# Performance work log

Hardware: AMD Instinct MI355X
Metric: run time of the kernel (lower is better)

The kernel has to match this reference:

```python
import jax, jax.numpy as jnp
import numpy as np

B, N, D = 1, 512, 128
KEEP = 0.75
LN_EPS = 1e-5


def _layer_norm(x, g, b):
    mu = jnp.mean(x, axis=-1, keepdims=True)
    var = jnp.mean(jnp.square(x - mu), axis=-1, keepdims=True)
    return (x - mu) * jax.lax.rsqrt(var + LN_EPS) * g + b


def _low_norm_dropout(x, keep_fraction=KEEP):
    # Zero features whose L2 norm over d is below the (1-keep) quantile.
    norms = jnp.linalg.norm(x, axis=-1, keepdims=True)  # [B,N,N,1]
    threshold = jnp.quantile(norms.reshape(-1), 1.0 - keep_fraction)
    mask = (norms >= threshold).astype(x.dtype)
    return x * mask / (keep_fraction + 1e-8)


def _linear(x, w):
    # torch nn.Linear (no bias): y = x @ W^T, W is [out, in]
    return jnp.einsum('bijd,od->bijo', x, w)


def setup_inputs() -> dict:
    key = jax.random.key(0)
    ks = jax.random.split(key, 8)
    scale = float(np.sqrt(6.0 / (2.0 * D)))  # xavier_uniform-ish std
    z = jax.random.normal(ks[0], (B, N, N, D), dtype=jnp.float32)
    w = lambda k: jax.random.uniform(k, (D, D), dtype=jnp.float32, minval=-scale, maxval=scale)
    return {
        'z': z,
        'ln_in_g': jnp.ones((D,), jnp.float32),
        'ln_in_b': jnp.zeros((D,), jnp.float32),
        'w_proj_a': w(ks[1]),
        'w_gate_a': w(ks[2]),
        'w_proj_b': w(ks[3]),
        'w_gate_b': w(ks[4]),
        'w_gate_out': w(ks[5]),
        'ln_out_g': jnp.ones((D,), jnp.float32),
        'ln_out_b': jnp.zeros((D,), jnp.float32),
        'w_proj_out': w(ks[6]),
    }


def reference(z, ln_in_g, ln_in_b, w_proj_a, w_gate_a, w_proj_b, w_gate_b,
              w_gate_out, ln_out_g, ln_out_b, w_proj_out):
    residual = z
    m = _layer_norm(z, ln_in_g, ln_in_b)
    a = jax.nn.sigmoid(_linear(m, w_gate_a)) * _linear(m, w_proj_a)
    b = jax.nn.sigmoid(_linear(m, w_gate_b)) * _linear(m, w_proj_b)
    a = _low_norm_dropout(a)
    b = _low_norm_dropout(b)
    # outgoing triangle update: contract over k axis
    t = jnp.einsum('bikd,bjkd->bijd', a, b)
    t = _layer_norm(t, ln_out_g, ln_out_b)
    gate = jax.nn.sigmoid(_linear(m, w_gate_out))
    out = gate * _linear(t, w_proj_out)
    return residual + out
```

## Files before the change

kernel.cpp:

```cpp
#include <hip/hip_runtime.h>
#include <hip/hip_fp16.h>

typedef unsigned int u32;
typedef unsigned short u16;
typedef __attribute__((ext_vector_type(8))) short short8;
typedef __attribute__((ext_vector_type(8))) _Float16 half8;
typedef __attribute__((ext_vector_type(4))) float f32x4;

#define NN (512*512)
#define RANK 65537u

#define L1A 0
#define L1B 1024
#define L2A 2048
#define L2B 6144
#define L3A 10240
#define L3B 11264
#define SEL1 12288
#define REM1 12290
#define SEL2 12292
#define REM2 12294
#define THRF 12296
#define HTOT 12298


__device__ __forceinline__ float bf2f(u16 h){ return __uint_as_float(((u32)h)<<16); }
__device__ __forceinline__ u16 f2bf(float f){
    u32 u = __float_as_uint(f);
    return (u16)((u + 0x7FFFu + ((u>>16)&1u)) >> 16);
}
__device__ __forceinline__ u16 f2bf_rz(float f){
    return (u16)(__float_as_uint(f) >> 16);
}
__device__ __forceinline__ u16 f2h(float f){ return __half_as_ushort(__float2half_rn(f)); }
__device__ __forceinline__ float h2f(u16 b){ return __half2float(__ushort_as_half(b)); }
__device__ __forceinline__ half8 as_h8(short8 x){ union{short8 s; half8 h;} u; u.s=x; return u.h; }
__device__ __forceinline__ float fsig(float x){ return 1.f/(1.f+__expf(-x)); }

__global__ void k0_init(const float* __restrict__ wga, const float* __restrict__ wpa,
                        const float* __restrict__ wgb, const float* __restrict__ wpb,
                        const float* __restrict__ wgo, const float* __restrict__ wpo,
                        u16* __restrict__ wprep, u32* __restrict__ h)
{
    const int i = blockIdx.x*blockDim.x + threadIdx.x;
    const int stride = gridDim.x*blockDim.x;
    for (int j = i; j < HTOT; j += stride) h[j] = 0;
    for (int j = i; j < 16384; j += stride) {
        const int o = j >> 7, c = j & 127;
        const int dj = (j & ~127) | ((((c>>3) ^ (o&7)) << 3)) | (c & 7);
        const float* ws[4] = {wga, wpa, wgb, wpb};
        #pragma unroll
        for (int L = 0; L < 4; ++L) {
            float x = ws[L][j];
            u16 hb = f2h(x);
            float hf = h2f(hb);
            wprep[(L*3+0)*16384 + dj] = hb;
            wprep[(L*3+1)*16384 + dj] = f2bf(x - hf);
            wprep[(L*3+2)*16384 + dj] = f2bf(hf);
        }
        wprep[12*16384 + dj] = f2h(wgo[j]);
        wprep[13*16384 + dj] = f2bf(wpo[j]);
    }
}

__global__ __launch_bounds__(256,2) void k2_fused(
    const float* __restrict__ z, const float* __restrict__ lng, const float* __restrict__ lnb,
    const u16* __restrict__ wp,
    u16* __restrict__ at, u16* __restrict__ bt,
    float* __restrict__ na, float* __restrict__ nb)
{
    __shared__ u16 smem[32768];
    u16* const s0 = smem;
    u16* const s1 = smem + 16384;
    const int tid = threadIdx.x;
    const int r0 = blockIdx.x * 128;
    const int lane = tid & 63;
    const int wid  = tid >> 6;

    #pragma unroll
    for (int pass = 0; pass < 2; ++pass) {
        const int rl = pass*64 + (tid>>2);
        const int q  = tid & 3;
        const float* zr = z + (size_t)(r0 + rl)*128;
        float v[32];
        float s = 0.f;
        #pragma unroll
        for (int j = 0; j < 8; ++j) {
            float4 f = *(const float4*)(zr + q*4 + j*16);
            v[j*4+0]=f.x; v[j*4+1]=f.y; v[j*4+2]=f.z; v[j*4+3]=f.w;
            s += f.x+f.y+f.z+f.w;
        }
        s += __shfl_xor(s,1); s += __shfl_xor(s,2);
        const float mu = s * (1.f/128.f);
        float vs = 0.f;
        #pragma unroll
        for (int e = 0; e < 32; ++e) { float d = v[e]-mu; vs += d*d; }
        vs += __shfl_xor(vs,1); vs += __shfl_xor(vs,2);
        const float x = vs*(1.f/128.f) + 1e-5f;
        float rstd = rsqrtf(x);
        rstd = rstd*(1.5f - 0.5f*x*rstd*rstd);
        #pragma unroll
        for (int j = 0; j < 8; ++j) {
            const int k = q*4 + j*16;
            float4 g4 = *(const float4*)(lng + k);
            float4 b4 = *(const float4*)(lnb + k);
            float m0 = (v[j*4+0]-mu)*rstd*g4.x + b4.x;
            float m1 = (v[j*4+1]-mu)*rstd*g4.y + b4.y;
            float m2 = (v[j*4+2]-mu)*rstd*g4.z + b4.z;
            float m3 = (v[j*4+3]-mu)*rstd*g4.w + b4.w;
            ushort4 ph, pl;
            ph.x = f2h(m0); pl.x = f2bf_rz(m0 - h2f(ph.x));
            ph.y = f2h(m1); pl.y = f2bf_rz(m1 - h2f(ph.y));
            ph.z = f2h(m2); pl.z = f2bf_rz(m2 - h2f(ph.z));
            ph.w = f2h(m3); pl.w = f2bf_rz(m3 - h2f(ph.w));
            const int blk = j*2 + (q>>1);
            const int addr = rl*128 + ((blk ^ (rl&7))*8) + (q&1)*4;
            *(ushort4*)&s0[addr] = ph;
            *(ushort4*)&s1[addr] = pl;
        }
    }
    __syncthreads();

    const int lrow = lane & 15, lkg = lane >> 4;
    const int rw   = wid * 32;

    short8 ah[2][4], al[2][4], ahb[2][4];
    #pragma unroll
    for (int m = 0; m < 2; ++m)
        #pragma unroll
        for (int ks = 0; ks < 4; ++ks) {
            const int row = rw + m*16 + lrow, blk = ks*4 + lkg;
            const int addr = row*128 + ((blk ^ (row&7))*8);
            ah[m][ks] = *(const short8*)&s0[addr];
            al[m][ks] = *(const short8*)&s1[addr];
            short8 c;
            #pragma unroll
            for (int e = 0; e < 8; ++e) c[e] = (short)f2bf_rz(h2f((u16)ah[m][ks][e]));
            ahb[m][ks] = c;
        }
    __syncthreads();

    f32x4 accG[2][8], accP[2][8];

    auto issue = [&](int buf, int slot){
        const char* src = (const char*)wp + (size_t)slot*32768 + wid*8192 + lane*16;
        u16* dst = smem + buf*16384 + wid*4096;
        #pragma unroll
        for (int i = 0; i < 8; ++i) {
            __builtin_amdgcn_global_load_lds((const u32*)(src + i*1024), (u32*)(dst + i*512), 16, 0, 0);
        }
    };
    auto passF16 = [&](f32x4 (&acc)[2][8], const u16* buf){
        #pragma unroll
        for (int ks = 0; ks < 4; ++ks) {
            const int blk = ks*4 + lkg;
            half8 a0 = as_h8(ah[0][ks]), a1 = as_h8(ah[1][ks]);
            #pragma unroll
            for (int n = 0; n < 8; ++n) {
                const int o = n*16 + lrow;
                half8 bF = as_h8(*(const short8*)&buf[o*128 + ((blk ^ (o&7))*8)]);
                acc[0][n] = __builtin_amdgcn_mfma_f32_16x16x32_f16(a0, bF, acc[0][n], 0,0,0);
                acc[1][n] = __builtin_amdgcn_mfma_f32_16x16x32_f16(a1, bF, acc[1][n], 0,0,0);
            }
        }
    };
    auto passBFhb = [&](f32x4 (&acc)[2][8], const u16* buf){
        #pragma unroll
        for (int ks = 0; ks < 4; ++ks) {
            const int blk = ks*4 + lkg;
            short8 a0 = ahb[0][ks], a1 = ahb[1][ks];
            #pragma unroll
            for (int n = 0; n < 8; ++n) {
                const int o = n*16 + lrow;
                short8 bF = *(const short8*)&buf[o*128 + ((blk ^ (o&7))*8)];
                acc[0][n] = __builtin_amdgcn_mfma_f32_16x16x32_bf16(a0, bF, acc[0][n], 0,0,0);
                acc[1][n] = __builtin_amdgcn_mfma_f32_16x16x32_bf16(a1, bF, acc[1][n], 0,0,0);
            }
        }
    };
    auto passBFal = [&](f32x4 (&acc)[2][8], const u16* buf){
        #pragma unroll
        for (int ks = 0; ks < 4; ++ks) {
            const int blk = ks*4 + lkg;
            short8 a0 = al[0][ks], a1 = al[1][ks];
            #pragma unroll
            for (int n = 0; n < 8; ++n) {
                const int o = n*16 + lrow;
                short8 bF = *(const short8*)&buf[o*128 + ((blk ^ (o&7))*8)];
                acc[0][n] = __builtin_amdgcn_mfma_f32_16x16x32_bf16(a0, bF, acc[0][n], 0,0,0);
                acc[1][n] = __builtin_amdgcn_mfma_f32_16x16x32_bf16(a1, bF, acc[1][n], 0,0,0);
            }
        }
    };
    auto epi = [&](u16* __restrict__ dst, float* __restrict__ nrm){
        float ns[2][4];
        #pragma unroll
        for (int m=0;m<2;++m){ ns[m][0]=0.f; ns[m][1]=0.f; ns[m][2]=0.f; ns[m][3]=0.f; }
        #pragma unroll
        for (int m = 0; m < 2; ++m) {
            const int rb = r0 + rw + m*16 + lkg*4;
            #pragma unroll
            for (int n = 0; n < 8; ++n) {
                const int o = n*16 + lrow;
                ushort4 pk;
                float av;
                av = accP[m][n][0] * fsig(accG[m][n][0]); ns[m][0]+=av*av; pk.x=f2bf(av);
                av = accP[m][n][1] * fsig(accG[m][n][1]); ns[m][1]+=av*av; pk.y=f2bf(av);
                av = accP[m][n][2] * fsig(accG[m][n][2]); ns[m][2]+=av*av; pk.z=f2bf(av);
                av = accP[m][n][3] * fsig(accG[m][n][3]); ns[m][3]+=av*av; pk.w=f2bf(av);
                *(ushort4*)&dst[(size_t)o*NN + rb] = pk;
            }
        }
        #pragma unroll
        for (int m = 0; m < 2; ++m)
            #pragma unroll
            for (int g = 0; g < 4; ++g) {
                float s = ns[m][g];
                s += __shfl_xor(s,1); s += __shfl_xor(s,2); s += __shfl_xor(s,4); s += __shfl_xor(s,8);
                if (lrow == 0) nrm[r0 + rw + m*16 + lkg*4 + g] = sqrtf(s);
            }
    };
    auto zacc = [&](f32x4 (&a)[2][8]){
        #pragma unroll
        for (int m=0;m<2;++m)
            #pragma unroll
            for (int n=0;n<8;++n) a[m][n] = (f32x4){0.f,0.f,0.f,0.f};
    };

    u16* const b0 = smem;
    u16* const b1 = smem + 16384;
    issue(0, 0);

#define K2_STEP(I, BODY)                                             \
    issue(((I)+1)&1, (I)+1);                                         \
    asm volatile("s_waitcnt vmcnt(8)" ::: "memory");                 \
    __builtin_amdgcn_sched_barrier(0);                               \
    __builtin_amdgcn_s_barrier();                                    \
    __builtin_amdgcn_s_setprio(1);                                   \
    BODY                                                             \
    __builtin_amdgcn_s_setprio(0);                                   \
    asm volatile("s_waitcnt lgkmcnt(0)" ::: "memory");               \
    __builtin_amdgcn_sched_barrier(0);                               \
    __builtin_amdgcn_s_barrier();

    K2_STEP(0,  { zacc(accG); passF16(accG, b0); })
    K2_STEP(1,  { passBFhb(accG, b1); })
    K2_STEP(2,  { passBFal(accG, b0); })
    K2_STEP(3,  { zacc(accP); passF16(accP, b1); })
    K2_STEP(4,  { passBFhb(accP, b0); })
    K2_STEP(5,  { passBFal(accP, b1); })
    epi(at, na);
    K2_STEP(6,  { zacc(accG); passF16(accG, b0); })
    K2_STEP(7,  { passBFhb(accG, b1); })
    K2_STEP(8,  { passBFal(accG, b0); })
    K2_STEP(9,  { zacc(accP); passF16(accP, b1); })
    K2_STEP(10, { passBFhb(accP, b0); })
    asm volatile("s_waitcnt vmcnt(0)" ::: "memory");
    __builtin_amdgcn_sched_barrier(0);
    __builtin_amdgcn_s_barrier();
    __builtin_amdgcn_s_setprio(1);
    passBFal(accP, b1);
    __builtin_amdgcn_s_setprio(0);
    epi(bt, nb);
#undef K2_STEP
}

__global__ __launch_bounds__(256) void khA(const float* __restrict__ na, const float* __restrict__ nb,
                                           u32* __restrict__ h)
{
    __shared__ u32 ha[1024], hb[1024];
    const int tid = threadIdx.x;
    #pragma unroll
    for (int j = tid; j < 1024; j += 256) { ha[j] = 0; hb[j] = 0; }
    __syncthreads();
    const int i = (blockIdx.x*256 + tid)*4;
    float4 va = *(const float4*)(na + i);
    float4 vb = *(const float4*)(nb + i);
    atomicAdd(&ha[__float_as_uint(va.x)>>22], 1u);
    atomicAdd(&ha[__float_as_uint(va.y)>>22], 1u);
    atomicAdd(&ha[__float_as_uint(va.z)>>22], 1u);
    atomicAdd(&ha[__float_as_uint(va.w)>>22], 1u);
    atomicAdd(&hb[__float_as_uint(vb.x)>>22], 1u);
    atomicAdd(&hb[__float_as_uint(vb.y)>>22], 1u);
    atomicAdd(&hb[__float_as_uint(vb.z)>>22], 1u);
    atomicAdd(&hb[__float_as_uint(vb.w)>>22], 1u);
    __syncthreads();
    #pragma unroll
    for (int j = tid; j < 1024; j += 256) {
        if (ha[j]) atomicAdd(&h[L1A + j], ha[j]);
        if (hb[j]) atomicAdd(&h[L1B + j], hb[j]);
    }
}

__device__ __forceinline__ void scan256s(u32* cum, int tid){
    for (int off = 1; off < 256; off <<= 1) {
        u32 tv = (tid >= off) ? cum[tid-off] : 0u;
        __syncthreads();
        cum[tid] += tv;
        __syncthreads();
    }
}

__global__ __launch_bounds__(256) void ksA(u32* __restrict__ h)
{
    __shared__ u32 cum[256];
    const int tid = threadIdx.x;
    for (int s2 = 0; s2 < 2; ++s2) {
        const u32* bins = h + (s2 ? L1B : L1A);
        u32 loc[4]; u32 s = 0;
        #pragma unroll
        for (int j = 0; j < 4; ++j) { loc[j] = bins[tid*4+j]; s += loc[j]; }
        cum[tid] = s;
        __syncthreads();
        scan256s(cum, tid);
        u32 prev = tid ? cum[tid-1] : 0u;
        if (cum[tid] >= RANK && prev < RANK) {
            u32 rem = RANK - prev;
            #pragma unroll
            for (int j = 0; j < 4; ++j) {
                if (rem <= loc[j]) { h[SEL1+s2] = (u32)(tid*4+j); h[REM1+s2] = rem; break; }
                rem -= loc[j];
            }
        }
        __syncthreads();
    }
}

__global__ __launch_bounds__(256) void khB(const float* __restrict__ na, const float* __restrict__ nb,
                                           u32* __restrict__ h)
{
    __shared__ u32 ha[4096], hb[4096];
    const int tid = threadIdx.x;
    #pragma unroll
    for (int j = tid; j < 4096; j += 256) { ha[j] = 0; hb[j] = 0; }
    const u32 c1a = h[SEL1+0], c1b = h[SEL1+1];
    __syncthreads();
    const int i = (blockIdx.x*256 + tid)*4;
    float4 va = *(const float4*)(na + i);
    float4 vb = *(const float4*)(nb + i);
    u32 u;
    u = __float_as_uint(va.x); if ((u>>22)==c1a) atomicAdd(&ha[(u>>10)&4095u],1u);
    u = __float_as_uint(va.y); if ((u>>22)==c1a) atomicAdd(&ha[(u>>10)&4095u],1u);
    u = __float_as_uint(va.z); if ((u>>22)==c1a) atomicAdd(&ha[(u>>10)&4095u],1u);
    u = __float_as_uint(va.w); if ((u>>22)==c1a) atomicAdd(&ha[(u>>10)&4095u],1u);
    u = __float_as_uint(vb.x); if ((u>>22)==c1b) atomicAdd(&hb[(u>>10)&4095u],1u);
    u = __float_as_uint(vb.y); if ((u>>22)==c1b) atomicAdd(&hb[(u>>10)&4095u],1u);
    u = __float_as_uint(vb.z); if ((u>>22)==c1b) atomicAdd(&hb[(u>>10)&4095u],1u);
    u = __float_as_uint(vb.w); if ((u>>22)==c1b) atomicAdd(&hb[(u>>10)&4095u],1u);
    __syncthreads();
    #pragma unroll
    for (int j = tid; j < 4096; j += 256) {
        if (ha[j]) atomicAdd(&h[L2A + j], ha[j]);
        if (hb[j]) atomicAdd(&h[L2B + j], hb[j]);
    }
}

__global__ __launch_bounds__(256) void ksB(u32* __restrict__ h)
{
    __shared__ u32 cum[256];
    const int tid = threadIdx.x;
    for (int s2 = 0; s2 < 2; ++s2) {
        const u32* bins = h + (s2 ? L2B : L2A);
        const u32 rank = h[REM1+s2];
        u32 loc[16]; u32 s = 0;
        #pragma unroll
        for (int j = 0; j < 16; ++j) { loc[j] = bins[tid*16+j]; s += loc[j]; }
        cum[tid] = s;
        __syncthreads();
        scan256s(cum, tid);
        u32 prev = tid ? cum[tid-1] : 0u;
        if (cum[tid] >= rank && prev < rank) {
            u32 rem = rank - prev;
            #pragma unroll
            for (int j = 0; j < 16; ++j) {
                if (rem <= loc[j]) {
                    h[SEL2+s2] = (h[SEL1+s2]<<12) | (u32)(tid*16+j);
                    h[REM2+s2] = rem;
                    break;
                }
                rem -= loc[j];
            }
        }
        __syncthreads();
    }
}

__global__ __launch_bounds__(256) void khC(const float* __restrict__ na, const float* __restrict__ nb,
                                           u32* __restrict__ h)
{
    __shared__ u32 ha[1024], hb[1024];
    const int tid = threadIdx.x;
    #pragma unroll
    for (int j = tid; j < 1024; j += 256) { ha[j] = 0; hb[j] = 0; }
    const u32 p2a = h[SEL2+0], p2b = h[SEL2+1];
    __syncthreads();
    const int i = (blockIdx.x*256 + tid)*4;
    float4 va = *(const float4*)(na + i);
    float4 vb = *(const float4*)(nb + i);
    u32 u;
    u = __float_as_uint(va.x); if ((u>>10)==p2a) atomicAdd(&ha[u&1023u],1u);
    u = __float_as_uint(va.y); if ((u>>10)==p2a) atomicAdd(&ha[u&1023u],1u);
    u = __float_as_uint(va.z); if ((u>>10)==p2a) atomicAdd(&ha[u&1023u],1u);
    u = __float_as_uint(va.w); if ((u>>10)==p2a) atomicAdd(&ha[u&1023u],1u);
    u = __float_as_uint(vb.x); if ((u>>10)==p2b) atomicAdd(&hb[u&1023u],1u);
    u = __float_as_uint(vb.y); if ((u>>10)==p2b) atomicAdd(&hb[u&1023u],1u);
    u = __float_as_uint(vb.z); if ((u>>10)==p2b) atomicAdd(&hb[u&1023u],1u);
    u = __float_as_uint(vb.w); if ((u>>10)==p2b) atomicAdd(&hb[u&1023u],1u);
    __syncthreads();
    #pragma unroll
    for (int j = tid; j < 1024; j += 256) {
        if (ha[j]) atomicAdd(&h[L3A + j], ha[j]);
        if (hb[j]) atomicAdd(&h[L3B + j], hb[j]);
    }
}

__global__ __launch_bounds__(256) void ksC(u32* __restrict__ h)
{
    __shared__ u32 cum[256];
    const int tid = threadIdx.x;
    for (int s2 = 0; s2 < 2; ++s2) {
        const u32* bins = h + (s2 ? L3B : L3A);
        const u32 rank = h[REM2+s2];
        u32 loc[4]; u32 s = 0;
        #pragma unroll
        for (int j = 0; j < 4; ++j) { loc[j] = bins[tid*4+j]; s += loc[j]; }
        cum[tid] = s;
        __syncthreads();
        scan256s(cum, tid);
        u32 prev = tid ? cum[tid-1] : 0u;
        if (cum[tid] >= rank && prev < rank) {
            u32 rem = rank - prev;
            #pragma unroll
            for (int j = 0; j < 4; ++j) {
                if (rem <= loc[j]) {
                    u32 key = (h[SEL2+s2]<<10) | (u32)(tid*4+j);
                    ((float*)(h + THRF))[s2] = __uint_as_float(key);
                    break;
                }
                rem -= loc[j];
            }
        }
        __syncthreads();
    }
}

__global__ __launch_bounds__(256) void k25(const float* __restrict__ na, const float* __restrict__ nb,
                                           const u32* __restrict__ h,
                                           u16* __restrict__ sa, u16* __restrict__ sb)
{
    const float* tf = (const float*)(h + THRF);
    const float ta = tf[0], tb = tf[1];
    const int i = (blockIdx.x*256 + threadIdx.x)*4;
    float4 va = *(const float4*)(na + i);
    float4 vb = *(const float4*)(nb + i);
    ushort4 ma, mb;
    ma.x = (va.x >= ta) ? 0xFFFFu : 0u;
    ma.y = (va.y >= ta) ? 0xFFFFu : 0u;
    ma.z = (va.z >= ta) ? 0xFFFFu : 0u;
    ma.w = (va.w >= ta) ? 0xFFFFu : 0u;
    mb.x = (vb.x >= tb) ? 0xFFFFu : 0u;
    mb.y = (vb.y >= tb) ? 0xFFFFu : 0u;
    mb.z = (vb.z >= tb) ? 0xFFFFu : 0u;
    mb.w = (vb.w >= tb) ? 0xFFFFu : 0u;
    *(ushort4*)&sa[i] = ma;
    *(ushort4*)&sb[i] = mb;
}

__global__ __launch_bounds__(256) void k3_einsum(
    const u16* __restrict__ at, const u16* __restrict__ bt,
    const u16* __restrict__ sa, const u16* __restrict__ sb,
    u16* __restrict__ tOut)
{
    __shared__ u16 aS[128*64];
    __shared__ u16 bS[128*64];
    const int tid = threadIdx.x;
    const int wg = blockIdx.x;
    const int xcd = wg & 7, idx = wg >> 3;
    const int d    = xcd*16 + (idx>>4);
    const int tile = idx & 15;
    const int i0 = (tile>>2)*128, j0 = (tile&3)*128;
    const u16* ap = at + (size_t)d*NN;
    const u16* bp = bt + (size_t)d*NN;

    const int lane = tid & 63, wid = tid >> 6;
    const int lrow = lane & 15, lkg = lane >> 4;
    const int wm = (wid>>1)*64, wn = (wid&1)*64;

    f32x4 acc[4][4];
    #pragma unroll
    for (int m=0;m<4;++m)
        #pragma unroll
        for (int n=0;n<4;++n) acc[m][n] = (f32x4){0.f,0.f,0.f,0.f};

    for (int kk = 0; kk < 8; ++kk) {
        const int k0 = kk*64;
        #pragma unroll
        for (int it = 0; it < 4; ++it) {
            const int b   = tid + it*256;
            const int row = b >> 3, k8 = b & 7;
            const int slot = ((k8 ^ (row&7))*8);
            {
                const int ga = (i0+row)*512 + k0 + k8*8;
                short8 x = *(const short8*)(ap + ga);
                short8 m = *(const short8*)(sa + ga);
                *(short8*)&aS[row*64 + slot] = x & m;
            }
            {
                const int gb = (j0+row)*512 + k0 + k8*8;
                short8 x = *(const short8*)(bp + gb);
                short8 m = *(const short8*)(sb + gb);
                *(short8*)&bS[row*64 + slot] = x & m;
            }
        }
        __syncthreads();
        #pragma unroll
        for (int ks = 0; ks < 2; ++ks) {
            const int blk = ks*4 + lkg;
            short8 aF[4], bF[4];
            #pragma unroll
            for (int m = 0; m < 4; ++m) {
                const int row = wm + m*16 + lrow;
                aF[m] = *(const short8*)&aS[row*64 + ((blk ^ (row&7))*8)];
            }
            #pragma unroll
            for (int n = 0; n < 4; ++n) {
                const int col = wn + n*16 + lrow;
                bF[n] = *(const short8*)&bS[col*64 + ((blk ^ (col&7))*8)];
            }
            #pragma unroll
            for (int m = 0; m < 4; ++m)
                #pragma unroll
                for (int n = 0; n < 4; ++n)
                    acc[m][n] = __builtin_amdgcn_mfma_f32_16x16x32_bf16(aF[m], bF[n], acc[m][n], 0,0,0);
        }
        __syncthreads();
    }
    u16* tp = tOut + (size_t)d*NN;
    #pragma unroll
    for (int m = 0; m < 4; ++m)
        #pragma unroll
        for (int n = 0; n < 4; ++n) {
            const int col = j0 + wn + n*16 + lrow;
            #pragma unroll
            for (int rg = 0; rg < 4; ++rg) {
                const int row = i0 + wm + m*16 + lkg*4 + rg;
                tp[row*512 + col] = f2bf(acc[m][n][rg]);
            }
        }
}

__global__ __launch_bounds__(256) void k4_final(
    const u16* __restrict__ t, const float* __restrict__ z,
    const float* __restrict__ lngI, const float* __restrict__ lnbI,
    const float* __restrict__ lngO, const float* __restrict__ lnbO,
    const u16* __restrict__ wprep, float* __restrict__ out)
{
    __shared__ u16 tS[128*128];
    __shared__ u16 wS[128*128];
    const int tid = threadIdx.x;
    const int r0 = blockIdx.x * 128;
    const int lane = tid & 63, wid = tid >> 6;
    const int lrow = lane & 15, lkg = lane >> 4;
    const int rw = wid * 32;

    {
        const int dd = tid>>1, hh = tid&1;
        const u16* tp = t + (size_t)dd*NN + r0 + hh*64;
        const int blk = dd >> 3, sub = dd & 7;
        #pragma unroll
        for (int jb = 0; jb < 8; ++jb) {
            short8 x = *(const short8*)(tp + jb*8);
            #pragma unroll
            for (int e = 0; e < 8; ++e) {
                const int r = hh*64 + jb*8 + e;
                tS[r*128 + ((blk ^ (r&7))*8) + sub] = (u16)x[e];
            }
        }
    }
    {
        const u16* wsrc = wprep + 13*16384;
        #pragma unroll
        for (int i = 0; i < 8; ++i)
            *(short8*)&wS[tid*64 + i*8] = *(const short8*)&wsrc[tid*64 + i*8];
    }
    __syncthreads();

    #pragma unroll
    for (int pass = 0; pass < 2; ++pass) {
        const int rl = pass*64 + (tid>>2);
        const int q  = tid & 3;
        float v[32]; float s = 0.f;
        #pragma unroll
        for (int j = 0; j < 8; ++j) {
            const int blk = j*2 + (q>>1);
            ushort4 x = *(const ushort4*)&tS[rl*128 + ((blk ^ (rl&7))*8) + (q&1)*4];
            float f0=bf2f(x.x), f1=bf2f(x.y), f2=bf2f(x.z), f3=bf2f(x.w);
            v[j*4+0]=f0; v[j*4+1]=f1; v[j*4+2]=f2; v[j*4+3]=f3;
            s += f0+f1+f2+f3;
        }
        s += __shfl_xor(s,1); s += __shfl_xor(s,2);
        const float mu = s * (1.f/128.f);
        float vs = 0.f;
        #pragma unroll
        for (int e = 0; e < 32; ++e) { float d = v[e]-mu; vs += d*d; }
        vs += __shfl_xor(vs,1); vs += __shfl_xor(vs,2);
        const float x = vs*(1.f/128.f) + 1e-5f;
        float rstd = rsqrtf(x);
        rstd = rstd*(1.5f - 0.5f*x*rstd*rstd);
        #pragma unroll
        for (int j = 0; j < 8; ++j) {
            const int k = q*4 + j*16;
            float4 g4 = *(const float4*)(lngO + k);
            float4 b4 = *(const float4*)(lnbO + k);
            ushort4 pk;
            pk.x = f2bf((v[j*4+0]-mu)*rstd*g4.x + b4.x);
            pk.y = f2bf((v[j*4+1]-mu)*rstd*g4.y + b4.y);
            pk.z = f2bf((v[j*4+2]-mu)*rstd*g4.z + b4.z);
            pk.w = f2bf((v[j*4+3]-mu)*rstd*g4.w + b4.w);
            const int blk = j*2 + (q>>1);
            *(ushort4*)&tS[rl*128 + ((blk ^ (rl&7))*8) + (q&1)*4] = pk;
        }
    }
    __syncthreads();

    f32x4 acc1[2][8];
    #pragma unroll
    for (int m=0;m<2;++m)
        #pragma unroll
        for (int n=0;n<8;++n) acc1[m][n] = (f32x4){0.f,0.f,0.f,0.f};
    #pragma unroll
    for (int ks = 0; ks < 4; ++ks) {
        const int blk = ks*4 + lkg;
        short8 aF[2];
        #pragma unroll
        for (int m = 0; m < 2; ++m) {
            const int row = rw + m*16 + lrow;
            aF[m] = *(const short8*)&tS[row*128 + ((blk ^ (row&7))*8)];
        }
        #pragma unroll
        for (int n = 0; n < 8; ++n) {
            const int o = n*16 + lrow;
            short8 bF = *(const short8*)&wS[o*128 + ((blk ^ (o&7))*8)];
            acc1[0][n] = __builtin_amdgcn_mfma_f32_16x16x32_bf16(aF[0], bF, acc1[0][n], 0,0,0);
            acc1[1][n] = __builtin_amdgcn_mfma_f32_16x16x32_bf16(aF[1], bF, acc1[1][n], 0,0,0);
        }
    }
    __syncthreads();

    {
        const u16* wsrc = wprep + 12*16384;
        #pragma unroll
        for (int i = 0; i < 8; ++i)
            *(short8*)&wS[tid*64 + i*8] = *(const short8*)&wsrc[tid*64 + i*8];
    }
    #pragma unroll
    for (int pass = 0; pass < 2; ++pass) {
        const int rl = pass*64 + (tid>>2);
        const int q  = tid & 3;
        const float* zr = z + (size_t)(r0 + rl)*128;
        float v[32]; float s = 0.f;
        #pragma unroll
        for (int j = 0; j < 8; ++j) {
            float4 f = *(const float4*)(zr + q*4 + j*16);
            v[j*4+0]=f.x; v[j*4+1]=f.y; v[j*4+2]=f.z; v[j*4+3]=f.w;
            s += f.x+f.y+f.z+f.w;
        }
        s += __shfl_xor(s,1); s += __shfl_xor(s,2);
        const float mu = s * (1.f/128.f);
        float vs = 0.f;
        #pragma unroll
        for (int e = 0; e < 32; ++e) { float d = v[e]-mu; vs += d*d; }
        vs += __shfl_xor(vs,1); vs += __shfl_xor(vs,2);
        const float x = vs*(1.f/128.f) + 1e-5f;
        float rstd = rsqrtf(x);
        rstd = rstd*(1.5f - 0.5f*x*rstd*rstd);
        #pragma unroll
        for (int j = 0; j < 8; ++j) {
            const int k = q*4 + j*16;
            float4 g4 = *(const float4*)(lngI + k);
            float4 b4 = *(const float4*)(lnbI + k);
            ushort4 ph;
            ph.x = f2h((v[j*4+0]-mu)*rstd*g4.x + b4.x);
            ph.y = f2h((v[j*4+1]-mu)*rstd*g4.y + b4.y);
            ph.z = f2h((v[j*4+2]-mu)*rstd*g4.z + b4.z);
            ph.w = f2h((v[j*4+3]-mu)*rstd*g4.w + b4.w);
            const int blk = j*2 + (q>>1);
            *(ushort4*)&tS[rl*128 + ((blk ^ (rl&7))*8) + (q&1)*4] = ph;
        }
    }
    __syncthreads();

    f32x4 acc2[2][8];
    #pragma unroll
    for (int m=0;m<2;++m)
        #pragma unroll
        for (int n=0;n<8;++n) acc2[m][n] = (f32x4){0.f,0.f,0.f,0.f};
    #pragma unroll
    for (int ks = 0; ks < 4; ++ks) {
        const int blk = ks*4 + lkg;
        half8 aF[2];
        #pragma unroll
        for (int m = 0; m < 2; ++m) {
            const int row = rw + m*16 + lrow;
            aF[m] = as_h8(*(const short8*)&tS[row*128 + ((blk ^ (row&7))*8)]);
        }
        #pragma unroll
        for (int n = 0; n < 8; ++n) {
            const int o = n*16 + lrow;
            half8 bF = as_h8(*(const short8*)&wS[o*128 + ((blk ^ (o&7))*8)]);
            acc2[0][n] = __builtin_amdgcn_mfma_f32_16x16x32_f16(aF[0], bF, acc2[0][n], 0,0,0);
            acc2[1][n] = __builtin_amdgcn_mfma_f32_16x16x32_f16(aF[1], bF, acc2[1][n], 0,0,0);
        }
    }

    #pragma unroll
    for (int m = 0; m < 2; ++m) {
        const int rb = r0 + rw + m*16 + lkg*4;
        #pragma unroll
        for (int n = 0; n < 8; ++n) {
            const int o = n*16 + lrow;
            #pragma unroll
            for (int j = 0; j < 4; ++j) {
                const size_t gidx = (size_t)(rb+j)*128 + o;
                float g = fsig(acc2[m][n][j]);
                out[gidx] = z[gidx] + g*acc1[m][n][j];
            }
        }
    }
}

extern "C" void kernel_launch(void* const* d_in, const int* in_sizes, int n_in,
                              void* d_out, int out_size, void* d_ws, size_t ws_size,
                              hipStream_t stream)
{
    const float* z    = (const float*)d_in[0];
    const float* lngI = (const float*)d_in[1];
    const float* lnbI = (const float*)d_in[2];
    const float* wpa  = (const float*)d_in[3];
    const float* wga  = (const float*)d_in[4];
    const float* wpb  = (const float*)d_in[5];
    const float* wgb  = (const float*)d_in[6];
    const float* wgo  = (const float*)d_in[7];
    const float* lngO = (const float*)d_in[8];
    const float* lnbO = (const float*)d_in[9];
    const float* wpo  = (const float*)d_in[10];
    float* out = (float*)d_out;

    char* ws = (char*)d_ws;
    u16*  at     = (u16*)(ws);
    u16*  bt     = (u16*)(ws + ((size_t)64<<20));
    u16*  sa     = (u16*)(ws + ((size_t)128<<20));
    u16*  sb     = (u16*)(ws + ((size_t)129<<20));
    u16*  t      = (u16*)(ws + ((size_t)192<<20));
    float* na    = (float*)(ws + ((size_t)256<<20));
    float* nb    = (float*)(ws + ((size_t)257<<20));
    u16*  wprep  = (u16*)(ws + ((size_t)258<<20));
    u32*  h      = (u32*)(ws + ((size_t)259<<20));

    hipLaunchKernelGGL(k0_init, dim3(512), dim3(256), 0, stream, wga, wpa, wgb, wpb, wgo, wpo, wprep, h);
    hipLaunchKernelGGL(k2_fused, dim3(2048), dim3(256), 0, stream, z, lngI, lnbI, wprep, at, bt, na, nb);
    hipLaunchKernelGGL(khA, dim3(256), dim3(256), 0, stream, na, nb, h);
    hipLaunchKernelGGL(ksA, dim3(1), dim3(256), 0, stream, h);
    hipLaunchKernelGGL(khB, dim3(256), dim3(256), 0, stream, na, nb, h);
    hipLaunchKernelGGL(ksB, dim3(1), dim3(256), 0, stream, h);
    hipLaunchKernelGGL(khC, dim3(256), dim3(256), 0, stream, na, nb, h);
    hipLaunchKernelGGL(ksC, dim3(1), dim3(256), 0, stream, h);
    hipLaunchKernelGGL(k25, dim3(256), dim3(256), 0, stream, na, nb, h, sa, sb);
    hipLaunchKernelGGL(k3_einsum, dim3(2048), dim3(256), 0, stream, at, bt, sa, sb, t);
    hipLaunchKernelGGL(k4_final, dim3(2048), dim3(256), 0, stream, t, z, lngI, lnbI, lngO, lnbO, wprep, out);
}
```

Measured before the change: 459.6 us.

## Fold quantile scan kernels into histogram consumers, add MFMA priority, vectorize transpose

Removes the three single-block scan kernels (ksA/ksB/ksC). Each consumer kernel now redoes the prefix scans of the needed histogram levels itself, so three serialized launches and their global round-trips go away. This costs redundant scan work in every block, up to six block-wide scans per block in k25. It also wraps the MFMA loops in s_setprio, and rewrites the t-tile load in k4 to read 8 short8 vectors per thread and transpose them in registers before 16-byte LDS stores, replacing scalar LDS writes.

Measured after the change: 516.5 us. 1.12x slower.

```diff
diff --git a/kernel.cpp b/kernel.cpp
--- a/kernel.cpp
+++ b/kernel.cpp
@@ -16,11 +16,6 @@
 #define L2B 6144
 #define L3A 10240
 #define L3B 11264
-#define SEL1 12288
-#define REM1 12290
-#define SEL2 12292
-#define REM2 12294
-#define THRF 12296
 #define HTOT 12298
 
 
@@ -265,6 +260,55 @@
 #undef K2_STEP
 }
 
+__device__ __forceinline__ void scan256s(u32* cum, int tid){
+    for (int off = 1; off < 256; off <<= 1) {
+        u32 tv = (tid >= off) ? cum[tid-off] : 0u;
+        __syncthreads();
+        cum[tid] += tv;
+        __syncthreads();
+    }
+}
+
+__device__ __forceinline__ void scanPick4(const u32* __restrict__ bins, u32 rank,
+                                          u32* cum, u32* shSel, u32* shRem, int tid){
+    u32 loc[4]; u32 s = 0;
+    #pragma unroll
+    for (int j = 0; j < 4; ++j) { loc[j] = bins[tid*4+j]; s += loc[j]; }
+    cum[tid] = s;
+    __syncthreads();
+    scan256s(cum, tid);
+    u32 prev = tid ? cum[tid-1] : 0u;
+    if (cum[tid] >= rank && prev < rank) {
+        u32 rem = rank - prev;
+        #pragma unroll
+        for (int j = 0; j < 4; ++j) {
+            if (rem <= loc[j]) { *shSel = (u32)(tid*4+j); *shRem = rem; break; }
+            rem -= loc[j];
+        }
+    }
+    __syncthreads();
+}
+
+__device__ __forceinline__ void scanPick16(const u32* __restrict__ bins, u32 rank,
+                                           u32* cum, u32* shSel, u32* shRem, int tid){
+    u32 loc[16]; u32 s = 0;
+    #pragma unroll
+    for (int j = 0; j < 16; ++j) { loc[j] = bins[tid*16+j]; s += loc[j]; }
+    cum[tid] = s;
+    __syncthreads();
+    scan256s(cum, tid);
+    u32 prev = tid ? cum[tid-1] : 0u;
+    if (cum[tid] >= rank && prev < rank) {
+        u32 rem = rank - prev;
+        #pragma unroll
+        for (int j = 0; j < 16; ++j) {
+            if (rem <= loc[j]) { *shSel = (u32)(tid*16+j); *shRem = rem; break; }
+            rem -= loc[j];
+        }
+    }
+    __syncthreads();
+}
+
 __global__ __launch_bounds__(256) void khA(const float* __restrict__ na, const float* __restrict__ nb,
                                            u32* __restrict__ h)
 {
@@ -292,48 +336,19 @@
     }
 }
 
-__device__ __forceinline__ void scan256s(u32* cum, int tid){
-    for (int off = 1; off < 256; off <<= 1) {
-        u32 tv = (tid >= off) ? cum[tid-off] : 0u;
-        __syncthreads();
-        cum[tid] += tv;
-        __syncthreads();
-    }
-}
-
-__global__ __launch_bounds__(256) void ksA(u32* __restrict__ h)
-{
-    __shared__ u32 cum[256];
-    const int tid = threadIdx.x;
-    for (int s2 = 0; s2 < 2; ++s2) {
-        const u32* bins = h + (s2 ? L1B : L1A);
-        u32 loc[4]; u32 s = 0;
-        #pragma unroll
-        for (int j = 0; j < 4; ++j) { loc[j] = bins[tid*4+j]; s += loc[j]; }
-        cum[tid] = s;
-        __syncthreads();
-        scan256s(cum, tid);
-        u32 prev = tid ? cum[tid-1] : 0u;
-        if (cum[tid] >= RANK && prev < RANK) {
-            u32 rem = RANK - prev;
-            #pragma unroll
-            for (int j = 0; j < 4; ++j) {
-                if (rem <= loc[j]) { h[SEL1+s2] = (u32)(tid*4+j); h[REM1+s2] = rem; break; }
-                rem -= loc[j];
-            }
-        }
-        __syncthreads();
-    }
-}
-
 __global__ __launch_bounds__(256) void khB(const float* __restrict__ na, const float* __restrict__ nb,
                                            u32* __restrict__ h)
 {
     __shared__ u32 ha[4096], hb[4096];
+    __shared__ u32 cum[256];
+    __shared__ u32 shS, shR;
     const int tid = threadIdx.x;
+    scanPick4(h + L1A, RANK, cum, &shS, &shR, tid);
+    const u32 c1a = shS;
+    scanPick4(h + L1B, RANK, cum, &shS, &shR, tid);
+    const u32 c1b = shS;
     #pragma unroll
     for (int j = tid; j < 4096; j += 256) { ha[j] = 0; hb[j] = 0; }
-    const u32 c1a = h[SEL1+0], c1b = h[SEL1+1];
     __syncthreads();
     const int i = (blockIdx.x*256 + tid)*4;
     float4 va = *(const float4*)(na + i);
@@ -355,44 +370,23 @@
     }
 }
 
-__global__ __launch_bounds__(256) void ksB(u32* __restrict__ h)
-{
-    __shared__ u32 cum[256];
-    const int tid = threadIdx.x;
-    for (int s2 = 0; s2 < 2; ++s2) {
-        const u32* bins = h + (s2 ? L2B : L2A);
-        const u32 rank = h[REM1+s2];
-        u32 loc[16]; u32 s = 0;
-        #pragma unroll
-        for (int j = 0; j < 16; ++j) { loc[j] = bins[tid*16+j]; s += loc[j]; }
-        cum[tid] = s;
-        __syncthreads();
-        scan256s(cum, tid);
-        u32 prev = tid ? cum[tid-1] : 0u;
-        if (cum[tid] >= rank && prev < rank) {
-            u32 rem = rank - prev;
-            #pragma unroll
-            for (int j = 0; j < 16; ++j) {
-                if (rem <= loc[j]) {
-                    h[SEL2+s2] = (h[SEL1+s2]<<12) | (u32)(tid*16+j);
-                    h[REM2+s2] = rem;
-                    break;
-                }
-                rem -= loc[j];
-            }
-        }
-        __syncthreads();
-    }
-}
-
 __global__ __launch_bounds__(256) void khC(const float* __restrict__ na, const float* __restrict__ nb,
                                            u32* __restrict__ h)
 {
     __shared__ u32 ha[1024], hb[1024];
+    __shared__ u32 cum[256];
+    __shared__ u32 shS, shR;
     const int tid = threadIdx.x;
+    scanPick4(h + L1A, RANK, cum, &shS, &shR, tid);
+    u32 s1 = shS, r1 = shR;
+    scanPick16(h + L2A, r1, cum, &shS, &shR, tid);
+    const u32 p2a = (s1<<12) | shS;
+    scanPick4(h + L1B, RANK, cum, &shS, &shR, tid);
+    s1 = shS; r1 = shR;
+    scanPick16(h + L2B, r1, cum, &shS, &shR, tid);
+    const u32 p2b = (s1<<12) | shS;
     #pragma unroll
     for (int j = tid; j < 1024; j += 256) { ha[j] = 0; hb[j] = 0; }
-    const u32 p2a = h[SEL2+0], p2b = h[SEL2+1];
     __syncthreads();
     const int i = (blockIdx.x*256 + tid)*4;
     float4 va = *(const float4*)(na + i);
@@ -414,43 +408,27 @@
     }
 }
 
-__global__ __launch_bounds__(256) void ksC(u32* __restrict__ h)
-{
-    __shared__ u32 cum[256];
-    const int tid = threadIdx.x;
-    for (int s2 = 0; s2 < 2; ++s2) {
-        const u32* bins = h + (s2 ? L3B : L3A);
-        const u32 rank = h[REM2+s2];
-        u32 loc[4]; u32 s = 0;
-        #pragma unroll
-        for (int j = 0; j < 4; ++j) { loc[j] = bins[tid*4+j]; s += loc[j]; }
-        cum[tid] = s;
-        __syncthreads();
-        scan256s(cum, tid);
-        u32 prev = tid ? cum[tid-1] : 0u;
-        if (cum[tid] >= rank && prev < rank) {
-            u32 rem = rank - prev;
-            #pragma unroll
-            for (int j = 0; j < 4; ++j) {
-                if (rem <= loc[j]) {
-                    u32 key = (h[SEL2+s2]<<10) | (u32)(tid*4+j);
-                    ((float*)(h + THRF))[s2] = __uint_as_float(key);
-                    break;
-                }
-                rem -= loc[j];
-            }
-        }
-        __syncthreads();
-    }
-}
-
 __global__ __launch_bounds__(256) void k25(const float* __restrict__ na, const float* __restrict__ nb,
                                            const u32* __restrict__ h,
                                            u16* __restrict__ sa, u16* __restrict__ sb)
 {
-    const float* tf = (const float*)(h + THRF);
-    const float ta = tf[0], tb = tf[1];
-    const int i = (blockIdx.x*256 + threadIdx.x)*4;
+    __shared__ u32 cum[256];
+    __shared__ u32 shS, shR;
+    const int tid = threadIdx.x;
+    scanPick4(h + L1A, RANK, cum, &shS, &shR, tid);
+    u32 s1 = shS, r1 = shR;
+    scanPick16(h + L2A, r1, cum, &shS, &shR, tid);
+    u32 s2 = (s1<<12) | shS, r2 = shR;
+    scanPick4(h + L3A, r2, cum, &shS, &shR, tid);
+    const float ta = __uint_as_float((s2<<10) | shS);
+    scanPick4(h + L1B, RANK, cum, &shS, &shR, tid);
+    s1 = shS; r1 = shR;
+    scanPick16(h + L2B, r1, cum, &shS, &shR, tid);
+    s2 = (s1<<12) | shS; r2 = shR;
+    scanPick4(h + L3B, r2, cum, &shS, &shR, tid);
+    const float tb = __uint_as_float((s2<<10) | shS);
+
+    const int i = (blockIdx.x*256 + tid)*4;
     float4 va = *(const float4*)(na + i);
     float4 vb = *(const float4*)(nb + i);
     ushort4 ma, mb;
@@ -513,6 +491,7 @@
             }
         }
         __syncthreads();
+        __builtin_amdgcn_s_setprio(1);
         #pragma unroll
         for (int ks = 0; ks < 2; ++ks) {
             const int blk = ks*4 + lkg;
@@ -533,6 +512,7 @@
                 for (int n = 0; n < 4; ++n)
                     acc[m][n] = __builtin_amdgcn_mfma_f32_16x16x32_bf16(aF[m], bF[n], acc[m][n], 0,0,0);
         }
+        __builtin_amdgcn_s_setprio(0);
         __syncthreads();
     }
     u16* tp = tOut + (size_t)d*NN;
@@ -564,17 +544,21 @@
     const int rw = wid * 32;
 
     {
-        const int dd = tid>>1, hh = tid&1;
-        const u16* tp = t + (size_t)dd*NN + r0 + hh*64;
-        const int blk = dd >> 3, sub = dd & 7;
-        #pragma unroll
-        for (int jb = 0; jb < 8; ++jb) {
-            short8 x = *(const short8*)(tp + jb*8);
-            #pragma unroll
-            for (int e = 0; e < 8; ++e) {
-                const int r = hh*64 + jb*8 + e;
-                tS[r*128 + ((blk ^ (r&7))*8) + sub] = (u16)x[e];
-            }
+        const int db  = tid & 15;
+        const int rb8 = tid >> 4;
+        short8 x[8];
+        #pragma unroll
+        for (int e = 0; e < 8; ++e) {
+            const int d = db*8 + e;
+            x[e] = *(const short8*)(t + (size_t)d*NN + r0 + rb8*8);
+        }
+        #pragma unroll
+        for (int rr = 0; rr < 8; ++rr) {
+            const int r = rb8*8 + rr;
+            short8 y;
+            #pragma unroll
+            for (int e = 0; e < 8; ++e) y[e] = x[e][rr];
+            *(short8*)&tS[r*128 + ((db ^ (r&7))*8)] = y;
         }
     }
     {
@@ -628,6 +612,7 @@
     for (int m=0;m<2;++m)
         #pragma unroll
         for (int n=0;n<8;++n) acc1[m][n] = (f32x4){0.f,0.f,0.f,0.f};
+    __builtin_amdgcn_s_setprio(1);
     #pragma unroll
     for (int ks = 0; ks < 4; ++ks) {
         const int blk = ks*4 + lkg;
@@ -645,6 +630,7 @@
             acc1[1][n] = __builtin_amdgcn_mfma_f32_16x16x32_bf16(aF[1], bF, acc1[1][n], 0,0,0);
         }
     }
+    __builtin_amdgcn_s_setprio(0);
     __syncthreads();
 
     {
@@ -695,6 +681,7 @@
     for (int m=0;m<2;++m)
         #pragma unroll
         for (int n=0;n<8;++n) acc2[m][n] = (f32x4){0.f,0.f,0.f,0.f};
+    __builtin_amdgcn_s_setprio(1);
     #pragma unroll
     for (int ks = 0; ks < 4; ++ks) {
         const int blk = ks*4 + lkg;
@@ -712,6 +699,7 @@
             acc2[1][n] = __builtin_amdgcn_mfma_f32_16x16x32_f16(aF[1], bF, acc2[1][n], 0,0,0);
         }
     }
+    __builtin_amdgcn_s_setprio(0);
 
     #pragma unroll
     for (int m = 0; m < 2; ++m) {
@@ -760,11 +748,8 @@
     hipLaunchKernelGGL(k0_init, dim3(512), dim3(256), 0, stream, wga, wpa, wgb, wpb, wgo, wpo, wprep, h);
     hipLaunchKernelGGL(k2_fused, dim3(2048), dim3(256), 0, stream, z, lngI, lnbI, wprep, at, bt, na, nb);
     hipLaunchKernelGGL(khA, dim3(256), dim3(256), 0, stream, na, nb, h);
-    hipLaunchKernelGGL(ksA, dim3(1), dim3(256), 0, stream, h);
     hipLaunchKernelGGL(khB, dim3(256), dim3(256), 0, stream, na, nb, h);
-    hipLaunchKernelGGL(ksB, dim3(1), dim3(256), 0, stream, h);
     hipLaunchKernelGGL(khC, dim3(256), dim3(256), 0, stream, na, nb, h);
-    hipLaunchKernelGGL(ksC, dim3(1), dim3(256), 0, stream, h);
     hipLaunchKernelGGL(k25, dim3(256), dim3(256), 0, stream, na, nb, h, sa, sb);
     hipLaunchKernelGGL(k3_einsum, dim3(2048), dim3(256), 0, stream, at, bt, sa, sb, t);
     hipLaunchKernelGGL(k4_final, dim3(2048), dim3(256), 0, stream, t, z, lngI, lnbI, lngO, lnbO, wprep, out);
```

## Deepen weight-tile prefetch in fused projection kernel to four LDS buffers

Applied to the files above, without the earlier changes.

Grows the shared-memory staging area of the fused LayerNorm+projection kernel from two to four 32 KB weight buffers. Weight slots are now prefetched two at a time and consumed in pairs per phase, which halves the number of barrier/wait rounds and keeps more global loads in flight. The cost is 128 KB of LDS per block, which likely limits the kernel to one resident block per CU instead of the two requested by its launch bounds. A few unused leftover pointer computations remain in the issue helper.

Result: slower. 537.9 us (+17.0%).

```diff
diff --git a/kernel.cpp b/kernel.cpp
--- a/kernel.cpp
+++ b/kernel.cpp
@@ -69,13 +69,13 @@
     u16* __restrict__ at, u16* __restrict__ bt,
     float* __restrict__ na, float* __restrict__ nb)
 {
-    __shared__ u16 smem[32768];
-    u16* const s0 = smem;
-    u16* const s1 = smem + 16384;
+    __shared__ u16 smem[65536];
     const int tid = threadIdx.x;
     const int r0 = blockIdx.x * 128;
     const int lane = tid & 63;
     const int wid  = tid >> 6;
+    u16* const s0 = smem;
+    u16* const s1 = smem + 16384;
 
     #pragma unroll
     for (int pass = 0; pass < 2; ++pass) {
@@ -142,12 +142,16 @@
 
     f32x4 accG[2][8], accP[2][8];
 
-    auto issue = [&](int buf, int slot){
+    auto issue = [&](int rb, int slot){
         const char* src = (const char*)wp + (size_t)slot*32768 + wid*8192 + lane*16;
-        u16* dst = smem + buf*16384 + wid*4096;
+        u16* dst = smem + rb*8192 + wid*2048;
+        dst = smem + rb*16384/2; (void)dst;
+        u16* d2 = smem + rb*16384 + wid*4096;
+        (void)d2;
+        u16* dreal = smem + (size_t)rb*16384 + wid*4096;
         #pragma unroll
         for (int i = 0; i < 8; ++i) {
-            __builtin_amdgcn_global_load_lds((const u32*)(src + i*1024), (u32*)(dst + i*512), 16, 0, 0);
+            __builtin_amdgcn_global_load_lds((const u32*)(src + i*1024), (u32*)(dreal + i*512), 16, 0, 0);
         }
     };
     auto passF16 = [&](f32x4 (&acc)[2][8], const u16* buf){
@@ -227,42 +231,41 @@
             for (int n=0;n<8;++n) a[m][n] = (f32x4){0.f,0.f,0.f,0.f};
     };
 
-    u16* const b0 = smem;
-    u16* const b1 = smem + 16384;
-    issue(0, 0);
-
-#define K2_STEP(I, BODY)                                             \
-    issue(((I)+1)&1, (I)+1);                                         \
-    asm volatile("s_waitcnt vmcnt(8)" ::: "memory");                 \
-    __builtin_amdgcn_sched_barrier(0);                               \
-    __builtin_amdgcn_s_barrier();                                    \
-    __builtin_amdgcn_s_setprio(1);                                   \
-    BODY                                                             \
-    __builtin_amdgcn_s_setprio(0);                                   \
-    asm volatile("s_waitcnt lgkmcnt(0)" ::: "memory");               \
-    __builtin_amdgcn_sched_barrier(0);                               \
+    u16* const rb0 = smem;
+    u16* const rb1 = smem + 16384;
+    u16* const rb2 = smem + 32768;
+    u16* const rb3 = smem + 49152;
+
+    issue(0, 0); issue(1, 1);
+
+#define K2_PHASE(SA, SB, RA, RB, BODYA, BODYB)                        \
+    issue(RA^2, SA+2); issue(RB^2, SB+2);                             \
+    asm volatile("s_waitcnt vmcnt(16)" ::: "memory");                 \
+    __builtin_amdgcn_sched_barrier(0);                                \
+    __builtin_amdgcn_s_barrier();                                     \
+    __builtin_amdgcn_s_setprio(1);                                    \
+    BODYA                                                             \
+    BODYB                                                             \
+    __builtin_amdgcn_s_setprio(0);                                    \
+    asm volatile("s_waitcnt lgkmcnt(0)" ::: "memory");                \
+    __builtin_amdgcn_sched_barrier(0);                                \
     __builtin_amdgcn_s_barrier();
 
-    K2_STEP(0,  { zacc(accG); passF16(accG, b0); })
-    K2_STEP(1,  { passBFhb(accG, b1); })
-    K2_STEP(2,  { passBFal(accG, b0); })
-    K2_STEP(3,  { zacc(accP); passF16(accP, b1); })
-    K2_STEP(4,  { passBFhb(accP, b0); })
-    K2_STEP(5,  { passBFal(accP, b1); })
+    K2_PHASE(0, 1, 0, 1, { zacc(accG); passF16(accG, rb0); }, { passBFhb(accG, rb1); })
+    K2_PHASE(2, 3, 2, 3, { passBFal(accG, rb2); }, { zacc(accP); passF16(accP, rb3); })
+    K2_PHASE(4, 5, 0, 1, { passBFhb(accP, rb0); }, { passBFal(accP, rb1); })
     epi(at, na);
-    K2_STEP(6,  { zacc(accG); passF16(accG, b0); })
-    K2_STEP(7,  { passBFhb(accG, b1); })
-    K2_STEP(8,  { passBFal(accG, b0); })
-    K2_STEP(9,  { zacc(accP); passF16(accP, b1); })
-    K2_STEP(10, { passBFhb(accP, b0); })
+    K2_PHASE(6, 7, 2, 3, { zacc(accG); passF16(accG, rb2); }, { passBFhb(accG, rb3); })
+    K2_PHASE(8, 9, 0, 1, { passBFal(accG, rb0); }, { zacc(accP); passF16(accP, rb1); })
     asm volatile("s_waitcnt vmcnt(0)" ::: "memory");
     __builtin_amdgcn_sched_barrier(0);
     __builtin_amdgcn_s_barrier();
     __builtin_amdgcn_s_setprio(1);
-    passBFal(accP, b1);
+    passBFhb(accP, rb2);
+    passBFal(accP, rb3);
     __builtin_amdgcn_s_setprio(0);
     epi(bt, nb);
-#undef K2_STEP
+#undef K2_PHASE
 }
 
 __global__ __launch_bounds__(256) void khA(const float* __restrict__ na, const float* __restrict__ nb,
```
